# Kernel tuning notes

Hardware: AMD Instinct MI355X
Metric: run time of the kernel (lower is better)

## Reference

```python
import jax, jax.numpy as jnp
import numpy as np

N, E, B = 30000, 360000, 8
FN, FE, D, L, M = 64, 16, 128, 3, 8
DK = D // M
NEG_SLOPE = 0.2
EPS = 1e-5


def setup_inputs() -> dict:
    key = jax.random.key(0)
    ks = jax.random.split(key, 24)
    rng = np.random.default_rng(0)
    Ng, Eg = N // B, E // B
    off = np.repeat(np.arange(B, dtype=np.int64) * Ng, Eg)
    src = jnp.asarray(rng.integers(0, Ng, size=E) + off, dtype=jnp.int32)
    dst = jnp.asarray(rng.integers(0, Ng, size=E) + off, dtype=jnp.int32)
    node_graph = jnp.asarray(np.repeat(np.arange(B), Ng), dtype=jnp.int32)
    edge_graph = jnp.asarray(np.repeat(np.arange(B), Eg), dtype=jnp.int32)
    p = lambda i, *s: jax.random.normal(ks[i], s, jnp.float32) * 0.05
    return dict(
        h=jax.random.normal(ks[0], (N, FN), jnp.float32),
        e=jax.random.normal(ks[1], (E, FE), jnp.float32),
        src=src, dst=dst, node_graph=node_graph, edge_graph=edge_graph,
        emb_n_w=p(2, D, FN), emb_n_b=p(3, D),
        emb_e_w=p(4, D, FE), emb_e_b=p(5, D),
        Us=p(6, L, D, D), Vs=p(7, L, D, D), As=p(8, L, D, D),
        Bs=p(9, L, D, D), Cs=p(10, L, D, D),
        gat_src_w=p(11, M * DK, D), gat_src_b=p(12, M * DK),
        gat_dst_w=p(13, M * DK, D), gat_dst_b=p(14, M * DK),
        gat_attn=p(15, M, DK), gat_bias=p(16, M * DK),
        O_w=p(17, D, D), O_b=p(18, D),
        W1_w=p(19, D, 3 * D), W1_b=p(20, D),
        W2_w=p(21, 1, D), W2_b=p(22, 1))


def _bn(x):
    # BatchNorm1d(affine=False), training mode: biased variance over batch dim
    return (x - x.mean(0)) * jax.lax.rsqrt(x.var(0) + EPS)


def reference(h, e, src, dst, node_graph, edge_graph,
              emb_n_w, emb_n_b, emb_e_w, emb_e_b,
              Us, Vs, As, Bs, Cs,
              gat_src_w, gat_src_b, gat_dst_w, gat_dst_b, gat_attn, gat_bias,
              O_w, O_b, W1_w, W1_b, W2_w, W2_b):
    h = h @ emb_n_w.T + emb_n_b  # [N, D]
    e = e @ emb_e_w.T + emb_e_b  # [E, D]
    for l in range(L):
        # u_mul_e('h','w','m') + max('m','agg'): gather-mul-segment_max
        m = (h @ Vs[l].T)[src] * jax.nn.sigmoid(e)  # [E, D]
        agg = jax.ops.segment_max(m, dst, num_segments=N)
        agg = jnp.where(jnp.isneginf(agg), 0.0, agg)  # DGL fills zero-in-degree with 0
        h_new = h + jax.nn.relu(_bn(h @ Us[l].T + agg))
        # inc('in')^T @ B(h) = B(h)[dst]; inc('out')^T @ C(h) = C(h)[src] (uses pre-update h)
        ee = (h @ Bs[l].T)[dst] + (h @ Cs[l].T)[src]
        e = e + jax.nn.relu(_bn(e @ As[l].T + ee))
        h = h_new
    # GATv2Conv(D, DK, M heads, allow_zero_in_degree=True)
    fs = (h @ gat_src_w.T + gat_src_b).reshape(N, M, DK)
    fd = (h @ gat_dst_w.T + gat_dst_b).reshape(N, M, DK)
    z = jax.nn.leaky_relu(fs[src] + fd[dst], NEG_SLOPE)  # [E, M, DK]
    score = jnp.einsum('emk,mk->em', z, gat_attn)        # [E, M]
    smax = jax.ops.segment_max(score, dst, num_segments=N)[dst]
    p = jnp.exp(score - smax)
    denom = jax.ops.segment_sum(p, dst, num_segments=N)[dst]
    a = p / denom
    rst = jax.ops.segment_sum(a[:, :, None] * fs[src], dst, num_segments=N)
    rst = rst + gat_bias.reshape(1, M, DK)
    h = rst.reshape(N, D) @ O_w.T + O_b
    # per-graph mean of node states, broadcast to that graph's edges
    cnt = jax.ops.segment_sum(jnp.ones((N,), h.dtype), node_graph, num_segments=B)
    moy = jax.ops.segment_sum(h, node_graph, num_segments=B) / cnt[:, None]
    out = jnp.concatenate([moy[edge_graph], h[src], h[dst]], axis=1)  # [E, 3D]
    out = jax.nn.relu(out @ W1_w.T + W1_b)
    out = out @ W2_w.T + W2_b
    return jax.nn.sigmoid(out)[:, 0]
```

## Files before the change

kernel.cpp:

```cpp
#include <hip/hip_runtime.h>

#define DF 128
#define NGRAPH 8

typedef __attribute__((ext_vector_type(8))) short bf16x8;
typedef __attribute__((ext_vector_type(4))) float f32x4;

__device__ __forceinline__ float sigm(float x) { return 1.f / (1.f + __expf(-x)); }
__device__ __forceinline__ unsigned short f2bf(float f) {
  unsigned u = __float_as_uint(f);
  u += 0x7FFFu + ((u >> 16) & 1u);
  return (unsigned short)(u >> 16);
}
__device__ __forceinline__ float bf2f(unsigned short u) {
  return __uint_as_float(((unsigned)u) << 16);
}
__device__ __forceinline__ float bflo(unsigned u) { return __uint_as_float(u << 16); }
__device__ __forceinline__ float bfhi(unsigned u) { return __uint_as_float(u & 0xffff0000u); }

__device__ __forceinline__ bf16x8 cvt8(const float* __restrict__ p) {
  float4 a = *(const float4*)p;
  float4 b = *(const float4*)(p + 4);
  bf16x8 r;
  r[0] = (short)f2bf(a.x); r[1] = (short)f2bf(a.y);
// ... 3 lines not shown
  return r;
}

__device__ __forceinline__ void agg_max(unsigned hv, unsigned ev, float& m0, float& m1) {
  m0 = fmaxf(m0, bflo(hv) * sigm(bflo(ev)));
  m1 = fmaxf(m1, bfhi(hv) * sigm(bfhi(ev)));
}

__global__ void k_fill_u32(unsigned* __restrict__ p, unsigned v, long long n) {
  long long i = (long long)blockIdx.x * blockDim.x + threadIdx.x;
  long long st = (long long)gridDim.x * blockDim.x;
  for (; i < n; i += st) p[i] = v;
}

__global__ void k_deg(const int* __restrict__ dst, unsigned* __restrict__ deg, int E) {
  int i = blockIdx.x * blockDim.x + threadIdx.x;
  int st = gridDim.x * blockDim.x;
  for (; i < E; i += st) atomicAdd(&deg[dst[i]], 1u);
}

__global__ __launch_bounds__(1024) void k_scan(
    const unsigned* __restrict__ deg, unsigned* __restrict__ rowptr,
    unsigned* __restrict__ cursor, int N) {
  __shared__ unsigned part[1024];
  int t = threadIdx.x;
  int per = (N + 1023) >> 10;
  int s0 = t * per, s1 = min(N, s0 + per);
  unsigned s = 0;
  for (int i = s0; i < s1; ++i) s += deg[i];
  part[t] = s;
  __syncthreads();
  for (int off = 1; off < 1024; off <<= 1) {
    unsigned v = (t >= off) ? part[t - off] : 0u;
    __syncthreads();
    part[t] += v;
    __syncthreads();
  }
  unsigned base = (t == 0) ? 0u : part[t - 1];
  for (int i = s0; i < s1; ++i) {
    rowptr[i] = base;
    cursor[i] = base;
    base += deg[i];
  }
  if (t == 1023) rowptr[N] = part[1023];
}

__global__ void k_scatter(const int* __restrict__ dst, unsigned* __restrict__ cursor,
                          int* __restrict__ eidb, int E) {
  int i = blockIdx.x * blockDim.x + threadIdx.x;
  int st = gridDim.x * blockDim.x;
  for (; i < E; i += st) {
    unsigned p = atomicAdd(&cursor[dst[i]], 1u);
    eidb[p] = i;
  }
}

__global__ __launch_bounds__(512) void k_wconv(
    const float* __restrict__ Us, const float* __restrict__ Vs,
    const float* __restrict__ As, const float* __restrict__ Bs,
    const float* __restrict__ Cs, const float* __restrict__ gsw,
    const float* __restrict__ gdw, const float* __restrict__ Ow,
    const float* __restrict__ W1, short* __restrict__ out) {
  int b = blockIdx.x;
  const float* W;
  int ldw = DF;
  if (b < 3) W = Us + b * 16384;
  else if (b < 6) W = Vs + (b - 3) * 16384;
  else if (b < 9) W = As + (b - 6) * 16384;
  else if (b < 12) W = Bs + (b - 9) * 16384;
  else if (b < 15) W = Cs + (b - 12) * 16384;
  else if (b == 15) W = gsw;
  else if (b == 16) W = gdw;
  else if (b == 17) W = Ow;
  else if (b == 18) { W = W1 + 128; ldw = 384; }
  else { W = W1 + 256; ldw = 384; }
  short* o = out + (size_t)b * 2048 * 8;
  for (int s = threadIdx.x; s < 2048; s += 512) {
    int ct = s >> 8, ks = (s >> 6) & 3, l = s & 63;
    int row = ct * 16 + (l & 15), k0 = ks * 32 + (l >> 4) * 8;
    *(bf16x8*)&o[s * 8] = cvt8(W + (size_t)row * ldw + k0);
  }
}

__global__ __launch_bounds__(128) void k_node_embed(
    const float* __restrict__ hin, const float* __restrict__ w,
    const float* __restrict__ b, float* __restrict__ h0, int rows) {
  __shared__ float Wt[64 * DF];
  __shared__ float ar[4][64];
  int tid = threadIdx.x;
  for (int i = tid; i < 64 * DF; i += 128) Wt[(i & 63) * DF + (i >> 6)] = w[i];
  float bb = b[tid];
  __syncthreads();
  for (int r0 = blockIdx.x * 4; r0 < rows; r0 += gridDim.x * 4) {
    for (int i = tid; i < 256; i += 128) ar[i >> 6][i & 63] = hin[(size_t)r0 * 64 + i];
    __syncthreads();
    float a0 = bb, a1 = bb, a2 = bb, a3 = bb;
#pragma unroll 8
    for (int k = 0; k < 64; ++k) {
      float wv = Wt[k * DF + tid];
      a0 = fmaf(ar[0][k], wv, a0); a1 = fmaf(ar[1][k], wv, a1);
      a2 = fmaf(ar[2][k], wv, a2); a3 = fmaf(ar[3][k], wv, a3);
    }
    h0[(size_t)r0 * DF + tid] = a0;
    h0[(size_t)(r0 + 1) * DF + tid] = a1;
    h0[(size_t)(r0 + 2) * DF + tid] = a2;
    h0[(size_t)(r0 + 3) * DF + tid] = a3;
    __syncthreads();
  }
}

__global__ __launch_bounds__(128) void k_edge_embed(
    const float* __restrict__ ein, const float* __restrict__ w,
    const float* __restrict__ b, unsigned short* __restrict__ e0u, int rows) {
  __shared__ float Wt[16 * DF];
  __shared__ float ar[4][16];
  int tid = threadIdx.x;
  for (int i = tid; i < 16 * DF; i += 128) Wt[(i & 15) * DF + (i >> 4)] = w[i];
  float bb = b[tid];
  __syncthreads();
  for (int r0 = blockIdx.x * 4; r0 < rows; r0 += gridDim.x * 4) {
    if (tid < 64) ar[tid >> 4][tid & 15] = ein[(size_t)r0 * 16 + tid];
    __syncthreads();
    float a0 = bb, a1 = bb, a2 = bb, a3 = bb;
#pragma unroll
    for (int k = 0; k < 16; ++k) {
      float wv = Wt[k * DF + tid];
      a0 = fmaf(ar[0][k], wv, a0); a1 = fmaf(ar[1][k], wv, a1);
      a2 = fmaf(ar[2][k], wv, a2); a3 = fmaf(ar[3][k], wv, a3);
    }
    e0u[(size_t)r0 * DF + tid] = f2bf(a0);
    e0u[(size_t)(r0 + 1) * DF + tid] = f2bf(a1);
    e0u[(size_t)(r0 + 2) * DF + tid] = f2bf(a2);
    e0u[(size_t)(r0 + 3) * DF + tid] = f2bf(a3);
    __syncthreads();
  }
}

template <int OUTBF>
__global__ __launch_bounds__(512) void k_gemm_mfma(
    const float* __restrict__ A, const short* __restrict__ Wf,
    const float* __restrict__ bias, void* __restrict__ outv, int rows) {
  __shared__ short Wb[2048 * 8];
  int tid = threadIdx.x;
  for (int s = tid; s < 2048; s += 512)
    *(bf16x8*)&Wb[s * 8] = *(const bf16x8*)&Wf[(size_t)s * 8];
  __syncthreads();
  float* outf = (float*)outv;
  unsigned short* outb = (unsigned short*)outv;
  int wid = tid >> 6, lane = tid & 63, q = lane >> 4, m = lane & 15;
  int ntiles = (rows + 127) >> 7;
  for (int t = blockIdx.x; t < ntiles; t += gridDim.x) {
    int r0 = t * 128 + wid * 16;
    int rr = r0 + m;
    if (rr >= rows) rr = rows - 1;
    const float* ap = A + (size_t)rr * DF + q * 8;
    bf16x8 a[4];
#pragma unroll
    for (int ks = 0; ks < 4; ++ks) a[ks] = cvt8(ap + 32 * ks);
#pragma unroll
    for (int ct = 0; ct < 8; ++ct) {
      f32x4 acc = {0.f, 0.f, 0.f, 0.f};
#pragma unroll
      for (int ks = 0; ks < 4; ++ks) {
        bf16x8 b = *(const bf16x8*)&Wb[((ct * 4 + ks) * 64 + lane) * 8];
        acc = __builtin_amdgcn_mfma_f32_16x16x32_bf16(a[ks], b, acc, 0, 0, 0);
      }
      int col = ct * 16 + m;
      float bb = bias ? bias[col] : 0.f;
#pragma unroll
      for (int j = 0; j < 4; ++j) {
        int row = r0 + q * 4 + j;
        if (row < rows) {
          if (OUTBF) outb[(size_t)row * DF + col] = f2bf(acc[j] + bb);
          else outf[(size_t)row * DF + col] = acc[j] + bb;
// ... 41 lines not shown

__global__ __launch_bounds__(512) void k_gemm4_mfma(
    const float* __restrict__ h0, const short* __restrict__ Vf,
    const short* __restrict__ Uf, const short* __restrict__ Bf,
    const short* __restrict__ Cf, unsigned short* __restrict__ hVb,
    float* __restrict__ hU, unsigned short* __restrict__ hBb,
    unsigned short* __restrict__ hCb, int rows) {
  __shared__ short Wl[4 * 2048 * 8];
  int tid = threadIdx.x;
  for (int s = tid; s < 2048; s += 512) {
    *(bf16x8*)&Wl[(size_t)s * 8] = *(const bf16x8*)&Vf[(size_t)s * 8];
    *(bf16x8*)&Wl[(size_t)(2048 + s) * 8] = *(const bf16x8*)&Uf[(size_t)s * 8];
    *(bf16x8*)&Wl[(size_t)(4096 + s) * 8] = *(const bf16x8*)&Bf[(size_t)s * 8];
    *(bf16x8*)&Wl[(size_t)(6144 + s) * 8] = *(const bf16x8*)&Cf[(size_t)s * 8];
  }
  __syncthreads();
  int wid = tid >> 6, lane = tid & 63, q = lane >> 4, m = lane & 15;
  int ntiles = (rows + 127) >> 7;
  for (int t = blockIdx.x; t < ntiles; t += gridDim.x) {
    int r0 = t * 128 + wid * 16;
    int rr = r0 + m;
    if (rr >= rows) rr = rows - 1;
    const float* ap = h0 + (size_t)rr * DF + q * 8;
    bf16x8 a[4];
#pragma unroll
    for (int ks = 0; ks < 4; ++ks) a[ks] = cvt8(ap + 32 * ks);
#pragma unroll
    for (int w = 0; w < 4; ++w) {
#pragma unroll
      for (int ct = 0; ct < 8; ++ct) {
        f32x4 acc = {0.f, 0.f, 0.f, 0.f};
#pragma unroll
        for (int ks = 0; ks < 4; ++ks) {
          bf16x8 b = *(const bf16x8*)&Wl[((w * 2048) + (ct * 4 + ks) * 64 + lane) * 8];
          acc = __builtin_amdgcn_mfma_f32_16x16x32_bf16(a[ks], b, acc, 0, 0, 0);
        }
        int col = ct * 16 + m;
#pragma unroll
        for (int j = 0; j < 4; ++j) {
          int row = r0 + q * 4 + j;
          if (row < rows) {
            if (w == 1) hU[(size_t)row * DF + col] = acc[j];
            else {
              unsigned short v = f2bf(acc[j]);
              unsigned short* o = (w == 0) ? hVb : ((w == 2) ? hBb : hCb);
              o[(size_t)row * DF + col] = v;
            }
          }
        }
      }
    }
  }
}


#define EDGE_MFMA_BODY                                                                 \
  const unsigned short* ep = e0u + (size_t)ec * DF + q * 8;                            \
  bf16x8 bv0 = *(const bf16x8*)(ep);                                                   \
  bf16x8 bv1 = *(const bf16x8*)(ep + 32);                                              \
  bf16x8 bv2 = *(const bf16x8*)(ep + 64);                                              \
  bf16x8 bv3 = *(const bf16x8*)(ep + 96);                                              \
  f32x4 c0 = {0.f, 0.f, 0.f, 0.f}, c1 = c0, c2 = c0, c3 = c0;                          \
  f32x4 c4 = c0, c5 = c0, c6 = c0, c7 = c0;                                            \
  _Pragma("unroll") for (int ks = 0; ks < 4; ++ks) {                                   \
    bf16x8 bv = (ks == 0) ? bv0 : (ks == 1) ? bv1 : (ks == 2) ? bv2 : bv3;             \
    c0 = __builtin_amdgcn_mfma_f32_16x16x32_bf16(*(const bf16x8*)&Wb[((0 * 4 + ks) * 64 + lane) * 8], bv, c0, 0, 0, 0); \
    c1 = __builtin_amdgcn_mfma_f32_16x16x32_bf16(*(const bf16x8*)&Wb[((1 * 4 + ks) * 64 + lane) * 8], bv, c1, 0, 0, 0); \
    c2 = __builtin_amdgcn_mfma_f32_16x16x32_bf16(*(const bf16x8*)&Wb[((2 * 4 + ks) * 64 + lane) * 8], bv, c2, 0, 0, 0); \
    c3 = __builtin_amdgcn_mfma_f32_16x16x32_bf16(*(const bf16x8*)&Wb[((3 * 4 + ks) * 64 + lane) * 8], bv, c3, 0, 0, 0); \
    c4 = __builtin_amdgcn_mfma_f32_16x16x32_bf16(*(const bf16x8*)&Wb[((4 * 4 + ks) * 64 + lane) * 8], bv, c4, 0, 0, 0); \
    c5 = __builtin_amdgcn_mfma_f32_16x16x32_bf16(*(const bf16x8*)&Wb[((5 * 4 + ks) * 64 + lane) * 8], bv, c5, 0, 0, 0); \
    c6 = __builtin_amdgcn_mfma_f32_16x16x32_bf16(*(const bf16x8*)&Wb[((6 * 4 + ks) * 64 + lane) * 8], bv, c6, 0, 0, 0); \
    c7 = __builtin_amdgcn_mfma_f32_16x16x32_bf16(*(const bf16x8*)&Wb[((7 * 4 + ks) * 64 + lane) * 8], bv, c7, 0, 0, 0); \
  }

__global__ __launch_bounds__(512) void k_edge_xs(
    const unsigned short* __restrict__ e0u, const short* __restrict__ Af,
    const unsigned short* __restrict__ hBb, const unsigned short* __restrict__ hCb,
    const int* __restrict__ src, const int* __restrict__ dst,
    float* __restrict__ stat, int Eg) {
  __shared__ short Wb[2048 * 8];
  __shared__ float ls[256];
  int tid = threadIdx.x;
  for (int s = tid; s < 2048; s += 512)
    *(bf16x8*)&Wb[s * 8] = *(const bf16x8*)&Af[(size_t)s * 8];
  if (tid < 256) ls[tid] = 0.f;
  int wid = tid >> 6, lane = tid & 63, q = lane >> 4, m = lane & 15;
  int g = blockIdx.x & 7, sub = blockIdx.x >> 3, nsub = gridDim.x >> 3;
  int gbase = g * Eg, gend = gbase + Eg;
  int tpg = (Eg + 127) >> 7;
  float ps[32], pq[32];
#pragma unroll
  for (int i = 0; i < 32; ++i) { ps[i] = 0.f; pq[i] = 0.f; }
  __syncthreads();
  for (int t = sub; t < tpg; t += nsub) {
    int r0 = gbase + t * 128 + wid * 16;
    int edge = r0 + m;
    bool ok = edge < gend;
    int ec = ok ? edge : gend - 1;
    EDGE_MFMA_BODY
    if (ok) {
      int sidx = src[ec], didx = dst[ec];
      const unsigned short* pb = hBb + (size_t)didx * DF + q * 4;
      const unsigned short* pc = hCb + (size_t)sidx * DF + q * 4;
#pragma unroll
      for (int ct = 0; ct < 8; ++ct) {
        f32x4 cc = (ct == 0) ? c0 : (ct == 1) ? c1 : (ct == 2) ? c2 : (ct == 3) ? c3
                   : (ct == 4) ? c4 : (ct == 5) ? c5 : (ct == 6) ? c6 : c7;
        ushort4 hb = *(const ushort4*)(pb + ct * 16);
        ushort4 hc = *(const ushort4*)(pc + ct * 16);
        float x0 = cc[0] + bf2f(hb.x) + bf2f(hc.x);
        float x1 = cc[1] + bf2f(hb.y) + bf2f(hc.y);
        float x2 = cc[2] + bf2f(hb.z) + bf2f(hc.z);
        float x3 = cc[3] + bf2f(hb.w) + bf2f(hc.w);
        ps[ct * 4 + 0] += x0; pq[ct * 4 + 0] += x0 * x0;
        ps[ct * 4 + 1] += x1; pq[ct * 4 + 1] += x1 * x1;
        ps[ct * 4 + 2] += x2; pq[ct * 4 + 2] += x2 * x2;
        ps[ct * 4 + 3] += x3; pq[ct * 4 + 3] += x3 * x3;
      }
    }
  }
#pragma unroll
  for (int i = 0; i < 32; ++i) {
    float s = ps[i], sq = pq[i];
    s += __shfl_xor(s, 1, 64); sq += __shfl_xor(sq, 1, 64);
    s += __shfl_xor(s, 2, 64); sq += __shfl_xor(sq, 2, 64);
    s += __shfl_xor(s, 4, 64); sq += __shfl_xor(sq, 4, 64);
    s += __shfl_xor(s, 8, 64); sq += __shfl_xor(sq, 8, 64);
    if (m == 0) {
      int feat = (i >> 2) * 16 + q * 4 + (i & 3);
      atomicAdd(&ls[feat], s);
      atomicAdd(&ls[128 + feat], sq);
    }
  }
  __syncthreads();
  if (tid < 128) {
    atomicAdd(&stat[512 + tid], ls[tid]);
    atomicAdd(&stat[640 + tid], ls[128 + tid]);
  }
}

__global__ __launch_bounds__(512) void k_edge_xa(
    unsigned short* __restrict__ e0u, const short* __restrict__ Af,
    const unsigned short* __restrict__ hBb, const unsigned short* __restrict__ hCb,
    const int* __restrict__ src, const int* __restrict__ dst,
    const float* __restrict__ stat, int Eg) {
  __shared__ short Wb[2048 * 8];
  int tid = threadIdx.x;
  for (int s = tid; s < 2048; s += 512)
    *(bf16x8*)&Wb[s * 8] = *(const bf16x8*)&Af[(size_t)s * 8];
  int wid = tid >> 6, lane = tid & 63, q = lane >> 4, m = lane & 15;
  float mm[32], iv[32];
#pragma unroll
  for (int ct = 0; ct < 8; ++ct)
#pragma unroll
    for (int j = 0; j < 4; ++j) {
      int f = ct * 16 + q * 4 + j;
      mm[ct * 4 + j] = stat[768 + f];
      iv[ct * 4 + j] = stat[896 + f];
    }
  int g = blockIdx.x & 7, sub = blockIdx.x >> 3, nsub = gridDim.x >> 3;
  int gbase = g * Eg, gend = gbase + Eg;
  int tpg = (Eg + 127) >> 7;
  __syncthreads();
  for (int t = sub; t < tpg; t += nsub) {
    int r0 = gbase + t * 128 + wid * 16;
    int edge = r0 + m;
    bool ok = edge < gend;
    int ec = ok ? edge : gend - 1;
    EDGE_MFMA_BODY
    if (ok) {
      int sidx = src[ec], didx = dst[ec];
      const unsigned short* pb = hBb + (size_t)didx * DF + q * 4;
      const unsigned short* pc = hCb + (size_t)sidx * DF + q * 4;
      unsigned short* pe = e0u + (size_t)ec * DF + q * 4;
#pragma unroll
      for (int ct = 0; ct < 8; ++ct) {
        f32x4 cc = (ct == 0) ? c0 : (ct == 1) ? c1 : (ct == 2) ? c2 : (ct == 3) ? c3
                   : (ct == 4) ? c4 : (ct == 5) ? c5 : (ct == 6) ? c6 : c7;
        ushort4 hb = *(const ushort4*)(pb + ct * 16);
        ushort4 hc = *(const ushort4*)(pc + ct * 16);
        ushort4 eo = *(const ushort4*)(pe + ct * 16);
        float x0 = cc[0] + bf2f(hb.x) + bf2f(hc.x);
        float x1 = cc[1] + bf2f(hb.y) + bf2f(hc.y);
        float x2 = cc[2] + bf2f(hb.z) + bf2f(hc.z);
        float x3 = cc[3] + bf2f(hb.w) + bf2f(hc.w);
        ushort4 nv;
        nv.x = f2bf(bf2f(eo.x) + fmaxf((x0 - mm[ct * 4 + 0]) * iv[ct * 4 + 0], 0.f));
        nv.y = f2bf(bf2f(eo.y) + fmaxf((x1 - mm[ct * 4 + 1]) * iv[ct * 4 + 1], 0.f));
        nv.z = f2bf(bf2f(eo.z) + fmaxf((x2 - mm[ct * 4 + 2]) * iv[ct * 4 + 2], 0.f));
        nv.w = f2bf(bf2f(eo.w) + fmaxf((x3 - mm[ct * 4 + 3]) * iv[ct * 4 + 3], 0.f));
        *(ushort4*)(pe + ct * 16) = nv;
      }
    }
  }
}

__global__ __launch_bounds__(256) void k_node_agg(
    float* __restrict__ hU, const unsigned short* __restrict__ hVb,
    const unsigned short* __restrict__ e0u, const int* __restrict__ src,
    const unsigned* __restrict__ rowptr, const int* __restrict__ eidb,
    float* __restrict__ stat, int Ngr) {
  __shared__ float sr[4][256];
  int tid = threadIdx.x, wid = tid >> 6, lane = tid & 63;
  int g = blockIdx.x & 7, sub = blockIdx.x >> 3, nsub = gridDim.x >> 3;
  float ps0 = 0.f, ps1 = 0.f, pq0 = 0.f, pq1 = 0.f;
  for (int nn = sub * 4 + wid; nn < Ngr; nn += nsub * 4) {
    int n = g * Ngr + nn;
    unsigned r0 = rowptr[n], r1 = rowptr[n + 1];
    float m0 = -3.4e38f, m1 = -3.4e38f;
    for (unsigned rc = r0; rc < r1; rc += 64) {
      int batch = (int)min(64u, r1 - rc);
      int myE = eidb[rc + ((lane < batch) ? lane : 0)];
      int myS = src[myE];
      int j = 0;
      for (; j + 4 <= batch; j += 4) {
        int e0 = __shfl(myE, j, 64), e1 = __shfl(myE, j + 1, 64);
        int e2 = __shfl(myE, j + 2, 64), e3 = __shfl(myE, j + 3, 64);
        int s0 = __shfl(myS, j, 64), s1 = __shfl(myS, j + 1, 64);
        int s2 = __shfl(myS, j + 2, 64), s3 = __shfl(myS, j + 3, 64);
        unsigned h0v = *(const unsigned*)&hVb[(size_t)s0 * DF + 2 * lane];
        unsigned h1v = *(const unsigned*)&hVb[(size_t)s1 * DF + 2 * lane];
        unsigned h2v = *(const unsigned*)&hVb[(size_t)s2 * DF + 2 * lane];
        unsigned h3v = *(const unsigned*)&hVb[(size_t)s3 * DF + 2 * lane];
        unsigned v0 = *(const unsigned*)&e0u[(size_t)e0 * DF + 2 * lane];
        unsigned v1 = *(const unsigned*)&e0u[(size_t)e1 * DF + 2 * lane];
        unsigned v2 = *(const unsigned*)&e0u[(size_t)e2 * DF + 2 * lane];
        unsigned v3 = *(const unsigned*)&e0u[(size_t)e3 * DF + 2 * lane];
        agg_max(h0v, v0, m0, m1);
        agg_max(h1v, v1, m0, m1);
        agg_max(h2v, v2, m0, m1);
        agg_max(h3v, v3, m0, m1);
      }
      for (; j < batch; ++j) {
        int e = __shfl(myE, j, 64);
        int s = __shfl(myS, j, 64);
        unsigned hv = *(const unsigned*)&hVb[(size_t)s * DF + 2 * lane];
        unsigned ev = *(const unsigned*)&e0u[(size_t)e * DF + 2 * lane];
        agg_max(hv, ev, m0, m1);
      }
    }
    if (r1 == r0) { m0 = 0.f; m1 = 0.f; }
    size_t idx = (size_t)n * DF + 2 * lane;
    float2 hu = *(float2*)&hU[idx];
    float t0 = hu.x + m0, t1 = hu.y + m1;
    hu.x = t0; hu.y = t1;
    *(float2*)&hU[idx] = hu;
    ps0 += t0; ps1 += t1;
    pq0 += t0 * t0; pq1 += t1 * t1;
  }
  sr[0][tid] = ps0; sr[1][tid] = ps1; sr[2][tid] = pq0; sr[3][tid] = pq1;
  __syncthreads();
  if (tid < 64) {
    float a0 = 0.f, a1 = 0.f, b0 = 0.f, b1 = 0.f;
#pragma unroll
    for (int w = 0; w < 4; ++w) {
      a0 += sr[0][w * 64 + tid]; a1 += sr[1][w * 64 + tid];
      b0 += sr[2][w * 64 + tid]; b1 += sr[3][w * 64 + tid];
    }
    atomicAdd(&stat[2 * tid], a0);
    atomicAdd(&stat[2 * tid + 1], a1);
    atomicAdd(&stat[128 + 2 * tid], b0);
    atomicAdd(&stat[128 + 2 * tid + 1], b1);
  }
}

__global__ void k_bn_finalize(float* __restrict__ stat, float nN, float nE) {
  int tid = threadIdx.x;
  if (tid < 128) {
    float mean = stat[tid] / nN;
    float var = stat[128 + tid] / nN - mean * mean;
    stat[256 + tid] = mean;
    stat[384 + tid] = rsqrtf(fmaxf(var, 0.f) + 1e-5f);
  } else {
    int d = tid - 128;
    float mean = stat[512 + d] / nE;
    float var = stat[640 + d] / nE - mean * mean;
    stat[768 + d] = mean;
    stat[896 + d] = rsqrtf(fmaxf(var, 0.f) + 1e-5f);
  }
}

__global__ __launch_bounds__(256) void k_node_update(
    float* __restrict__ h0, const float* __restrict__ hU,
    const float* __restrict__ stat, long long total) {
  long long i = (long long)blockIdx.x * blockDim.x + threadIdx.x;
  long long st = (long long)gridDim.x * blockDim.x;
  for (; i < total; i += st) {
    int d = (int)(i & 127);
    float t = (hU[i] - stat[256 + d]) * stat[384 + d];
    h0[i] += fmaxf(t, 0.f);
  }
}

__global__ __launch_bounds__(256) void k_gat_score(
    const unsigned short* __restrict__ fsb, const unsigned short* __restrict__ fdb,
    const int* __restrict__ src, const int* __restrict__ dst,
    const float* __restrict__ attn, float* __restrict__ score, int Eg) {
  int g = blockIdx.x & 7, sub = blockIdx.x >> 3, nsub = gridDim.x >> 3;
  int gbase = g * Eg, gend = gbase + Eg;
  int tpg = (Eg + 127) >> 7;
  int tid = threadIdx.x;
  for (int t = sub; t < tpg; t += nsub) {
    int ebase = gbase + t * 128;
    for (int k = tid; k < 1024; k += 256) {
      int e = ebase + (k >> 3);
      if (e >= gend) break;
      int mh = k & 7;
      int s = src[e], dn = dst[e];
      const unsigned short* ps = fsb + (size_t)s * DF + mh * 16;
      const unsigned short* pd = fdb + (size_t)dn * DF + mh * 16;
      const float* pa = attn + mh * 16;
      bf16x8 s0 = *(const bf16x8*)ps;
      bf16x8 s1 = *(const bf16x8*)(ps + 8);
      bf16x8 d0 = *(const bf16x8*)pd;
      bf16x8 d1 = *(const bf16x8*)(pd + 8);
      float acc = 0.f;
#pragma unroll
      for (int kk = 0; kk < 8; ++kk) {
        float z = bf2f((unsigned short)s0[kk]) + bf2f((unsigned short)d0[kk]);
        z = (z > 0.f) ? z : 0.2f * z;
        acc = fmaf(z, pa[kk], acc);
        float z2 = bf2f((unsigned short)s1[kk]) + bf2f((unsigned short)d1[kk]);
        z2 = (z2 > 0.f) ? z2 : 0.2f * z2;
        acc = fmaf(z2, pa[kk + 8], acc);
      }
      score[(size_t)e * 8 + mh] = acc;
    }
  }
}

__global__ __launch_bounds__(256) void k_gat_node(
    const float* __restrict__ score, const unsigned short* __restrict__ fsb,
    const int* __restrict__ src, const unsigned* __restrict__ rowptr,
    const int* __restrict__ eidb, float* __restrict__ rst, int Ngr) {
  int tid = threadIdx.x, wid = tid >> 6, lane = tid & 63;
  int g = blockIdx.x & 7, sub = blockIdx.x >> 3, nsub = gridDim.x >> 3;
  int head = lane >> 3, slot = lane & 7;
  for (int nn = sub * 4 + wid; nn < Ngr; nn += nsub * 4) {
    int n = g * Ngr + nn;
    unsigned r0 = rowptr[n], r1 = rowptr[n + 1];
    float hm = -3.4e38f;
    for (unsigned rc = r0; rc < r1; rc += 64) {
      int batch = (int)min(64u, r1 - rc);
      int myE = eidb[rc + ((lane < batch) ? lane : 0)];
      for (int k = slot; k < batch; k += 8) {
        int e = __shfl(myE, k, 64);
        hm = fmaxf(hm, score[(size_t)e * 8 + head]);
      }
    }
#pragma unroll
    for (int mk = 1; mk < 8; mk <<= 1) hm = fmaxf(hm, __shfl_xor(hm, mk, 64));
    float dn = 0.f;
    for (unsigned rc = r0; rc < r1; rc += 64) {
      int batch = (int)min(64u, r1 - rc);
      int myE = eidb[rc + ((lane < batch) ? lane : 0)];
      for (int k = slot; k < batch; k += 8) {
        int e = __shfl(myE, k, 64);
        dn += __expf(score[(size_t)e * 8 + head] - hm);
      }
    }
#pragma unroll
    for (int mk = 1; mk < 8; mk <<= 1) dn += __shfl_xor(dn, mk, 64);
    float inv = (r1 > r0) ? 1.f / dn : 0.f;
    float a0 = 0.f, a1 = 0.f;
    for (unsigned rc = r0; rc < r1; rc += 64) {
      int batch = (int)min(64u, r1 - rc);
      int myE = eidb[rc + ((lane < batch) ? lane : 0)];
      int myS = src[myE];
      int j = 0;
      for (; j + 4 <= batch; j += 4) {
        int e0 = __shfl(myE, j, 64), e1 = __shfl(myE, j + 1, 64);
        int e2 = __shfl(myE, j + 2, 64), e3 = __shfl(myE, j + 3, 64);
        int s0 = __shfl(myS, j, 64), s1 = __shfl(myS, j + 1, 64);
        int s2 = __shfl(myS, j + 2, 64), s3 = __shfl(myS, j + 3, 64);
        float sc0 = score[(size_t)e0 * 8 + head];
        float sc1 = score[(size_t)e1 * 8 + head];
        float sc2 = score[(size_t)e2 * 8 + head];
        float sc3 = score[(size_t)e3 * 8 + head];
        unsigned f0 = *(const unsigned*)&fsb[(size_t)s0 * DF + 2 * lane];
        unsigned f1 = *(const unsigned*)&fsb[(size_t)s1 * DF + 2 * lane];
        unsigned f2 = *(const unsigned*)&fsb[(size_t)s2 * DF + 2 * lane];
        unsigned f3 = *(const unsigned*)&fsb[(size_t)s3 * DF + 2 * lane];
        float w0 = __expf(sc0 - hm) * inv, w1 = __expf(sc1 - hm) * inv;
        float w2 = __expf(sc2 - hm) * inv, w3 = __expf(sc3 - hm) * inv;
        a0 = fmaf(w0, bflo(f0), a0); a1 = fmaf(w0, bfhi(f0), a1);
        a0 = fmaf(w1, bflo(f1), a0); a1 = fmaf(w1, bfhi(f1), a1);
        a0 = fmaf(w2, bflo(f2), a0); a1 = fmaf(w2, bfhi(f2), a1);
        a0 = fmaf(w3, bflo(f3), a0); a1 = fmaf(w3, bfhi(f3), a1);
      }
      for (; j < batch; ++j) {
        int e = __shfl(myE, j, 64);
        int s = __shfl(myS, j, 64);
        float w = __expf(score[(size_t)e * 8 + head] - hm) * inv;
        unsigned fv = *(const unsigned*)&fsb[(size_t)s * DF + 2 * lane];
        a0 = fmaf(w, bflo(fv), a0);
        a1 = fmaf(w, bfhi(fv), a1);
      }
    }
    float2 o;
    o.x = a0; o.y = a1;
    *(float2*)&rst[(size_t)n * DF + 2 * lane] = o;
  }
}

__global__ void k_bias2(const float* __restrict__ gat_bias,
                        const float* __restrict__ O_w,
                        const float* __restrict__ O_b, float* __restrict__ bias2) {
  int d = threadIdx.x;
  float acc = O_b[d];
  for (int k = 0; k < DF; ++k) acc = fmaf(gat_bias[k], O_w[(size_t)d * DF + k], acc);
  bias2[d] = acc;
}

__global__ __launch_bounds__(128) void k_moy(
    const unsigned short* __restrict__ h2b, const int* __restrict__ ng,
    float* __restrict__ moy, float* __restrict__ cnt, int rows) {
  int tid = threadIdx.x;
  int per = (rows + gridDim.x - 1) / gridDim.x;
  int n0 = blockIdx.x * per;
  int n1 = min(rows, n0 + per);
  if (n0 >= n1) return;
  int cur = ng[n0];
  float acc = 0.f; int c = 0;
  for (int n = n0; n < n1; ++n) {
    int g = ng[n];
    if (g != cur) {
      atomicAdd(&moy[cur * DF + tid], acc);
      if (tid == 0) atomicAdd(&cnt[cur], (float)c);
      acc = 0.f; c = 0; cur = g;
    }
    acc += bf2f(h2b[(size_t)n * DF + tid]);
    ++c;
  }
  atomicAdd(&moy[cur * DF + tid], acc);
  if (tid == 0) atomicAdd(&cnt[cur], (float)c);
}

__global__ void k_p0(const float* __restrict__ W1, const float* __restrict__ W1b_,
                     const float* __restrict__ moy, const float* __restrict__ cnt,
                     float* __restrict__ P0) {
  int g = blockIdx.x, d = threadIdx.x;
  float inv = 1.f / cnt[g];
  float acc = W1b_[d];
  for (int k = 0; k < DF; ++k) acc = fmaf(W1[(size_t)d * 384 + k], moy[g * DF + k] * inv, acc);
  P0[g * DF + d] = acc;
}

__global__ __launch_bounds__(256) void k_head(
    const unsigned short* __restrict__ P1b, const unsigned short* __restrict__ P2b,
    const float* __restrict__ P0, const int* __restrict__ src,
    const unsigned* __restrict__ rowptr, const int* __restrict__ eidb,
    const float* __restrict__ W2, const float* __restrict__ W2b,
    float* __restrict__ out, int Ngr) {
  int tid = threadIdx.x, wid = tid >> 6, lane = tid & 63;
  int g = blockIdx.x & 7, sub = blockIdx.x >> 3, nsub = gridDim.x >> 3;
  float w2b = W2b[0];
  float w20 = W2[2 * lane], w21 = W2[2 * lane + 1];
  float b0 = P0[g * DF + 2 * lane], b1v = P0[g * DF + 2 * lane + 1];
  for (int nn = sub * 4 + wid; nn < Ngr; nn += nsub * 4) {
    int n = g * Ngr + nn;
    unsigned r0 = rowptr[n], r1 = rowptr[n + 1];
    if (r1 == r0) continue;
    unsigned p2 = *(const unsigned*)&P2b[(size_t)n * DF + 2 * lane];
    float base0 = b0 + bflo(p2);
    float base1 = b1v + bfhi(p2);
    for (unsigned rc = r0; rc < r1; rc += 64) {
      int cnt2 = (int)min(64u, r1 - rc);
      int myE = eidb[rc + ((lane < cnt2) ? lane : 0)];
      int myS = src[myE];
      int j = 0;
      for (; j + 4 <= cnt2; j += 4) {
        int e0 = __shfl(myE, j, 64), e1 = __shfl(myE, j + 1, 64);
        int e2 = __shfl(myE, j + 2, 64), e3 = __shfl(myE, j + 3, 64);
        int s0 = __shfl(myS, j, 64), s1 = __shfl(myS, j + 1, 64);
        int s2 = __shfl(myS, j + 2, 64), s3 = __shfl(myS, j + 3, 64);
        unsigned u0 = *(const unsigned*)&P1b[(size_t)s0 * DF + 2 * lane];
        unsigned u1 = *(const unsigned*)&P1b[(size_t)s1 * DF + 2 * lane];
        unsigned u2 = *(const unsigned*)&P1b[(size_t)s2 * DF + 2 * lane];
        unsigned u3 = *(const unsigned*)&P1b[(size_t)s3 * DF + 2 * lane];
        float v0 = fmaxf(base0 + bflo(u0), 0.f) * w20 + fmaxf(base1 + bfhi(u0), 0.f) * w21;
        float v1 = fmaxf(base0 + bflo(u1), 0.f) * w20 + fmaxf(base1 + bfhi(u1), 0.f) * w21;
        float v2 = fmaxf(base0 + bflo(u2), 0.f) * w20 + fmaxf(base1 + bfhi(u2), 0.f) * w21;
        float v3 = fmaxf(base0 + bflo(u3), 0.f) * w20 + fmaxf(base1 + bfhi(u3), 0.f) * w21;
#pragma unroll
        for (int mk = 1; mk < 64; mk <<= 1) {
          v0 += __shfl_xor(v0, mk, 64);
          v1 += __shfl_xor(v1, mk, 64);
          v2 += __shfl_xor(v2, mk, 64);
          v3 += __shfl_xor(v3, mk, 64);
        }
        if (lane == 0) {
          out[e0] = sigm(v0 + w2b);
          out[e1] = sigm(v1 + w2b);
          out[e2] = sigm(v2 + w2b);
          out[e3] = sigm(v3 + w2b);
        }
      }
      for (; j < cnt2; ++j) {
        int e = __shfl(myE, j, 64);
        int s = __shfl(myS, j, 64);
        unsigned p1 = *(const unsigned*)&P1b[(size_t)s * DF + 2 * lane];
        float v = fmaxf(base0 + bflo(p1), 0.f) * w20 + fmaxf(base1 + bfhi(p1), 0.f) * w21;
#pragma unroll
        for (int mk = 1; mk < 64; mk <<= 1) v += __shfl_xor(v, mk, 64);
        if (lane == 0) out[e] = sigm(v + w2b);
      }
    }
  }
}

extern "C" void kernel_launch(void* const* d_in, const int* in_sizes, int n_in,
                              void* d_out, int out_size, void* d_ws, size_t ws_size,
                              hipStream_t stream) {
  const float* h_in = (const float*)d_in[0];
  const float* e_in = (const float*)d_in[1];
  const int* src = (const int*)d_in[2];
  const int* dst = (const int*)d_in[3];
  const int* node_graph = (const int*)d_in[4];
  const float* emb_n_w = (const float*)d_in[6];
  const float* emb_n_b = (const float*)d_in[7];
  const float* emb_e_w = (const float*)d_in[8];
  const float* emb_e_b = (const float*)d_in[9];
  const float* Us = (const float*)d_in[10];
  const float* Vs = (const float*)d_in[11];
  const float* As = (const float*)d_in[12];
  const float* Bs = (const float*)d_in[13];
  const float* Cs = (const float*)d_in[14];
  const float* gat_src_w = (const float*)d_in[15];
  const float* gat_src_b = (const float*)d_in[16];
  const float* gat_dst_w = (const float*)d_in[17];
  const float* gat_dst_b = (const float*)d_in[18];
  const float* gat_attn = (const float*)d_in[19];
  const float* gat_bias = (const float*)d_in[20];
  const float* O_w = (const float*)d_in[21];
  const float* O_b = (const float*)d_in[22];
  const float* W1_w = (const float*)d_in[23];
  const float* W1_b = (const float*)d_in[24];
  const float* W2_w = (const float*)d_in[25];
  const float* W2_b = (const float*)d_in[26];
  float* out = (float*)d_out;

  const int N = in_sizes[0] / 64;
  const int E = in_sizes[1] / 16;
  const int Eg = E / NGRAPH;
  const int Ngr = N / NGRAPH;

  auto rnd = [](size_t b) { return (b + 255) & ~(size_t)255; };
  const size_t sz_e0 = rnd((size_t)E * DF * 2);
  const size_t sz_node = rnd((size_t)N * DF * 4);
  const size_t sz_nodeb = rnd((size_t)N * DF * 2);
  const size_t sz_score = rnd((size_t)E * 8 * 4);
  const size_t sz_wfrag = rnd(20 * 2048 * 8 * 2);
  const size_t sz_rp = rnd((size_t)(N + 1) * 4);
  const size_t sz_eid = rnd((size_t)E * 4);
  const size_t sz_misc = rnd(4096 * 4);
  const size_t needed = sz_e0 + 3 * sz_node + 4 * sz_nodeb + sz_score + sz_wfrag +
                        3 * sz_rp + sz_eid + sz_misc;
  if (ws_size < needed) {
    k_fill_u32<<<256, 256, 0, stream>>>((unsigned*)out, 0xBF800000u, (long long)out_size);
    return;
  }

  char* wp = (char*)d_ws;
  auto alloc = [&](size_t bytes) { void* p = wp; wp += bytes; return p; };
  unsigned short* e0u = (unsigned short*)alloc(sz_e0);
  float* h0 = (float*)alloc(sz_node);
  float* hU = (float*)alloc(sz_node);
  float* rst = (float*)alloc(sz_node);
  unsigned short* hVb = (unsigned short*)alloc(sz_nodeb);
  unsigned short* hBb = (unsigned short*)alloc(sz_nodeb);
  unsigned short* hCb = (unsigned short*)alloc(sz_nodeb);
  unsigned short* h2b = (unsigned short*)alloc(sz_nodeb);
  float* score = (float*)alloc(sz_score);
  short* wfrag = (short*)alloc(sz_wfrag);
  unsigned* rowptr = (unsigned*)alloc(sz_rp);
  unsigned* cursor = (unsigned*)alloc(sz_rp);
  unsigned* deg = (unsigned*)alloc(sz_rp);
  int* eidb = (int*)alloc(sz_eid);
  float* misc = (float*)alloc(sz_misc);
  float* stat = misc;
  float* bias2 = misc + 1024;
  float* moy = misc + 1152;
  float* cnt = misc + 2176;
  float* P0 = misc + 2304;
  unsigned short* P1b = e0u;
  unsigned short* P2b = e0u + (size_t)N * DF;

  auto WF = [&](int idx) { return wfrag + (size_t)idx * 2048 * 8; };

  k_fill_u32<<<64, 256, 0, stream>>>(deg, 0u, N);
  k_deg<<<512, 256, 0, stream>>>(dst, deg, E);
  k_scan<<<1, 1024, 0, stream>>>(deg, rowptr, cursor, N);
  k_scatter<<<512, 256, 0, stream>>>(dst, cursor, eidb, E);

  k_wconv<<<20, 512, 0, stream>>>(Us, Vs, As, Bs, Cs, gat_src_w, gat_dst_w, O_w,
                                  W1_w, wfrag);

  const int gN = (N + 127) / 128;
  k_node_embed<<<2048, 128, 0, stream>>>(h_in, emb_n_w, emb_n_b, h0, N);
  k_edge_embed<<<4096, 128, 0, stream>>>(e_in, emb_e_w, emb_e_b, e0u, E);

  for (int l = 0; l < 3; ++l) {
    k_gemm4_mfma<<<gN, 512, 0, stream>>>(h0, WF(3 + l), WF(l), WF(9 + l), WF(12 + l),
                                         hVb, hU, hBb, hCb, N);
    k_fill_u32<<<4, 256, 0, stream>>>((unsigned*)stat, 0u, 1024);
    k_node_agg<<<2048, 256, 0, stream>>>(hU, hVb, e0u, src, rowptr, eidb, stat, Ngr);
    k_edge_xs<<<1024, 512, 0, stream>>>(e0u, WF(6 + l), hBb, hCb, src, dst, stat, Eg);
    k_bn_finalize<<<1, 256, 0, stream>>>(stat, (float)N, (float)E);
    k_node_update<<<2048, 256, 0, stream>>>(h0, hU, stat, (long long)N * DF);
    k_edge_xa<<<1024, 512, 0, stream>>>(e0u, WF(6 + l), hBb, hCb, src, dst, stat, Eg);
  }

  k_gemm_mfma<1><<<gN, 512, 0, stream>>>(h0, WF(15), gat_src_b, hVb, N);
  k_gemm_mfma<1><<<gN, 512, 0, stream>>>(h0, WF(16), gat_dst_b, hBb, N);
  k_gat_score<<<512, 256, 0, stream>>>(hVb, hBb, src, dst, gat_attn, score, Eg);
  k_gat_node<<<2048, 256, 0, stream>>>(score, hVb, src, rowptr, eidb, rst, Ngr);
  k_bias2<<<1, 128, 0, stream>>>(gat_bias, O_w, O_b, bias2);
  k_gemm_mfma<1><<<gN, 512, 0, stream>>>(rst, WF(17), bias2, h2b, N);

  k_fill_u32<<<2, 256, 0, stream>>>((unsigned*)moy, 0u, 1032);
  k_moy<<<128, 128, 0, stream>>>(h2b, node_graph, moy, cnt, N);
  k_p0<<<8, 128, 0, stream>>>(W1_w, W1_b, moy, cnt, P0);
  k_gemmb_mfma<<<gN, 512, 0, stream>>>(h2b, WF(18), P1b, N);
  k_gemmb_mfma<<<gN, 512, 0, stream>>>(h2b, WF(19), P2b, N);
  k_head<<<2048, 256, 0, stream>>>(P1b, P2b, P0, src, rowptr, eidb, W2_w, W2_b,
                                   out, Ngr);
}
```

Baseline: 1.473 ms.

## Store edge state in destination-sorted order with permuted src/dst indices

Edge embeddings are now written in CSR (destination-sorted) order, and permuted src/dst index arrays are built once, so the node aggregation, GAT softmax and edge kernels read edge data contiguously instead of through the eidb indirection. This removes a random gather per edge in node_agg and gat_node, and the GAT score kernel is flattened into a simple grid-stride loop. The cost is one extra permutation kernel, two more index buffers, and a gathered read of the raw edge features during embedding. Per-graph edge ranges still hold because edges stay within their graph after sorting.

```diff
diff --git a/kernel.cpp b/kernel.cpp
--- a/kernel.cpp
+++ b/kernel.cpp
@@ -79,6 +79,18 @@
   for (; i < E; i += st) {
     unsigned p = atomicAdd(&cursor[dst[i]], 1u);
     eidb[p] = i;
+  }
+}
+
+__global__ void k_permidx(const int* __restrict__ eidb, const int* __restrict__ src,
+                          const int* __restrict__ dst, int* __restrict__ srcP,
+                          int* __restrict__ dstP, int E) {
+  int i = blockIdx.x * blockDim.x + threadIdx.x;
+  int st = gridDim.x * blockDim.x;
+  for (; i < E; i += st) {
+    int e = eidb[i];
+    srcP[i] = src[e];
+    dstP[i] = dst[e];
   }
 }
 
@@ -137,8 +149,9 @@
 }
 
 __global__ __launch_bounds__(128) void k_edge_embed(
-    const float* __restrict__ ein, const float* __restrict__ w,
-    const float* __restrict__ b, unsigned short* __restrict__ e0u, int rows) {
+    const float* __restrict__ ein, const int* __restrict__ eidb,
+    const float* __restrict__ w, const float* __restrict__ b,
+    unsigned short* __restrict__ e0u, int rows) {
   __shared__ float Wt[16 * DF];
   __shared__ float ar[4][16];
   int tid = threadIdx.x;
@@ -146,7 +159,10 @@
   float bb = b[tid];
   __syncthreads();
   for (int r0 = blockIdx.x * 4; r0 < rows; r0 += gridDim.x * 4) {
-    if (tid < 64) ar[tid >> 4][tid & 15] = ein[(size_t)r0 * 16 + tid];
+    if (tid < 64) {
+      int e = eidb[r0 + (tid >> 4)];
+      ar[tid >> 4][tid & 15] = ein[(size_t)e * 16 + (tid & 15)];
+    }
     __syncthreads();
     float a0 = bb, a1 = bb, a2 = bb, a3 = bb;
 #pragma unroll
@@ -294,7 +310,6 @@
     }
   }
 }
-
 
 #define EDGE_MFMA_BODY                                                                 \
   const unsigned short* ep = e0u + (size_t)ec * DF + q * 8;                            \
@@ -319,7 +334,7 @@
 __global__ __launch_bounds__(512) void k_edge_xs(
     const unsigned short* __restrict__ e0u, const short* __restrict__ Af,
     const unsigned short* __restrict__ hBb, const unsigned short* __restrict__ hCb,
-    const int* __restrict__ src, const int* __restrict__ dst,
+    const int* __restrict__ srcP, const int* __restrict__ dstP,
     float* __restrict__ stat, int Eg) {
   __shared__ short Wb[2048 * 8];
   __shared__ float ls[256];
@@ -342,7 +357,7 @@
     int ec = ok ? edge : gend - 1;
     EDGE_MFMA_BODY
     if (ok) {
-      int sidx = src[ec], didx = dst[ec];
+      int sidx = srcP[ec], didx = dstP[ec];
       const unsigned short* pb = hBb + (size_t)didx * DF + q * 4;
       const unsigned short* pc = hCb + (size_t)sidx * DF + q * 4;
 #pragma unroll
@@ -385,7 +400,7 @@
 __global__ __launch_bounds__(512) void k_edge_xa(
     unsigned short* __restrict__ e0u, const short* __restrict__ Af,
     const unsigned short* __restrict__ hBb, const unsigned short* __restrict__ hCb,
-    const int* __restrict__ src, const int* __restrict__ dst,
+    const int* __restrict__ srcP, const int* __restrict__ dstP,
     const float* __restrict__ stat, int Eg) {
   __shared__ short Wb[2048 * 8];
   int tid = threadIdx.x;
@@ -412,7 +427,7 @@
     int ec = ok ? edge : gend - 1;
     EDGE_MFMA_BODY
     if (ok) {
-      int sidx = src[ec], didx = dst[ec];
+      int sidx = srcP[ec], didx = dstP[ec];
       const unsigned short* pb = hBb + (size_t)didx * DF + q * 4;
       const unsigned short* pc = hCb + (size_t)sidx * DF + q * 4;
       unsigned short* pe = e0u + (size_t)ec * DF + q * 4;
@@ -440,9 +455,8 @@
 
 __global__ __launch_bounds__(256) void k_node_agg(
     float* __restrict__ hU, const unsigned short* __restrict__ hVb,
-    const unsigned short* __restrict__ e0u, const int* __restrict__ src,
-    const unsigned* __restrict__ rowptr, const int* __restrict__ eidb,
-    float* __restrict__ stat, int Ngr) {
+    const unsigned short* __restrict__ e0u, const int* __restrict__ srcP,
+    const unsigned* __restrict__ rowptr, float* __restrict__ stat, int Ngr) {
   __shared__ float sr[4][256];
   int tid = threadIdx.x, wid = tid >> 6, lane = tid & 63;
   int g = blockIdx.x & 7, sub = blockIdx.x >> 3, nsub = gridDim.x >> 3;
@@ -453,32 +467,28 @@
     float m0 = -3.4e38f, m1 = -3.4e38f;
     for (unsigned rc = r0; rc < r1; rc += 64) {
       int batch = (int)min(64u, r1 - rc);
-      int myE = eidb[rc + ((lane < batch) ? lane : 0)];
-      int myS = src[myE];
+      int myS = srcP[rc + ((lane < batch) ? lane : 0)];
       int j = 0;
       for (; j + 4 <= batch; j += 4) {
-        int e0 = __shfl(myE, j, 64), e1 = __shfl(myE, j + 1, 64);
-        int e2 = __shfl(myE, j + 2, 64), e3 = __shfl(myE, j + 3, 64);
         int s0 = __shfl(myS, j, 64), s1 = __shfl(myS, j + 1, 64);
         int s2 = __shfl(myS, j + 2, 64), s3 = __shfl(myS, j + 3, 64);
         unsigned h0v = *(const unsigned*)&hVb[(size_t)s0 * DF + 2 * lane];
         unsigned h1v = *(const unsigned*)&hVb[(size_t)s1 * DF + 2 * lane];
         unsigned h2v = *(const unsigned*)&hVb[(size_t)s2 * DF + 2 * lane];
         unsigned h3v = *(const unsigned*)&hVb[(size_t)s3 * DF + 2 * lane];
-        unsigned v0 = *(const unsigned*)&e0u[(size_t)e0 * DF + 2 * lane];
-        unsigned v1 = *(const unsigned*)&e0u[(size_t)e1 * DF + 2 * lane];
-        unsigned v2 = *(const unsigned*)&e0u[(size_t)e2 * DF + 2 * lane];
-        unsigned v3 = *(const unsigned*)&e0u[(size_t)e3 * DF + 2 * lane];
+        unsigned v0 = *(const unsigned*)&e0u[(size_t)(rc + j) * DF + 2 * lane];
+        unsigned v1 = *(const unsigned*)&e0u[(size_t)(rc + j + 1) * DF + 2 * lane];
+        unsigned v2 = *(const unsigned*)&e0u[(size_t)(rc + j + 2) * DF + 2 * lane];
+        unsigned v3 = *(const unsigned*)&e0u[(size_t)(rc + j + 3) * DF + 2 * lane];
         agg_max(h0v, v0, m0, m1);
         agg_max(h1v, v1, m0, m1);
         agg_max(h2v, v2, m0, m1);
         agg_max(h3v, v3, m0, m1);
       }
       for (; j < batch; ++j) {
-        int e = __shfl(myE, j, 64);
         int s = __shfl(myS, j, 64);
         unsigned hv = *(const unsigned*)&hVb[(size_t)s * DF + 2 * lane];
-        unsigned ev = *(const unsigned*)&e0u[(size_t)e * DF + 2 * lane];
+        unsigned ev = *(const unsigned*)&e0u[(size_t)(rc + j) * DF + 2 * lane];
         agg_max(hv, ev, m0, m1);
       }
     }
@@ -537,45 +547,39 @@
 
 __global__ __launch_bounds__(256) void k_gat_score(
     const unsigned short* __restrict__ fsb, const unsigned short* __restrict__ fdb,
-    const int* __restrict__ src, const int* __restrict__ dst,
-    const float* __restrict__ attn, float* __restrict__ score, int Eg) {
-  int g = blockIdx.x & 7, sub = blockIdx.x >> 3, nsub = gridDim.x >> 3;
-  int gbase = g * Eg, gend = gbase + Eg;
-  int tpg = (Eg + 127) >> 7;
-  int tid = threadIdx.x;
-  for (int t = sub; t < tpg; t += nsub) {
-    int ebase = gbase + t * 128;
-    for (int k = tid; k < 1024; k += 256) {
-      int e = ebase + (k >> 3);
-      if (e >= gend) break;
-      int mh = k & 7;
-      int s = src[e], dn = dst[e];
-      const unsigned short* ps = fsb + (size_t)s * DF + mh * 16;
-      const unsigned short* pd = fdb + (size_t)dn * DF + mh * 16;
-      const float* pa = attn + mh * 16;
-      bf16x8 s0 = *(const bf16x8*)ps;
-      bf16x8 s1 = *(const bf16x8*)(ps + 8);
-      bf16x8 d0 = *(const bf16x8*)pd;
-      bf16x8 d1 = *(const bf16x8*)(pd + 8);
-      float acc = 0.f;
-#pragma unroll
-      for (int kk = 0; kk < 8; ++kk) {
-        float z = bf2f((unsigned short)s0[kk]) + bf2f((unsigned short)d0[kk]);
-        z = (z > 0.f) ? z : 0.2f * z;
-        acc = fmaf(z, pa[kk], acc);
-        float z2 = bf2f((unsigned short)s1[kk]) + bf2f((unsigned short)d1[kk]);
-        z2 = (z2 > 0.f) ? z2 : 0.2f * z2;
-        acc = fmaf(z2, pa[kk + 8], acc);
-      }
-      score[(size_t)e * 8 + mh] = acc;
-    }
+    const int* __restrict__ srcP, const int* __restrict__ dstP,
+    const float* __restrict__ attn, float* __restrict__ score, int E) {
+  long long i = (long long)blockIdx.x * blockDim.x + threadIdx.x;
+  long long st = (long long)gridDim.x * blockDim.x;
+  long long total = (long long)E * 8;
+  for (; i < total; i += st) {
+    int e = (int)(i >> 3), mh = (int)(i & 7);
+    int s = srcP[e], dn = dstP[e];
+    const unsigned short* ps = fsb + (size_t)s * DF + mh * 16;
+    const unsigned short* pd = fdb + (size_t)dn * DF + mh * 16;
+    const float* pa = attn + mh * 16;
+    bf16x8 s0 = *(const bf16x8*)ps;
+    bf16x8 s1 = *(const bf16x8*)(ps + 8);
+    bf16x8 d0 = *(const bf16x8*)pd;
+    bf16x8 d1 = *(const bf16x8*)(pd + 8);
+    float acc = 0.f;
+#pragma unroll
+    for (int kk = 0; kk < 8; ++kk) {
+      float z = bf2f((unsigned short)s0[kk]) + bf2f((unsigned short)d0[kk]);
+      z = (z > 0.f) ? z : 0.2f * z;
+      acc = fmaf(z, pa[kk], acc);
+      float z2 = bf2f((unsigned short)s1[kk]) + bf2f((unsigned short)d1[kk]);
+      z2 = (z2 > 0.f) ? z2 : 0.2f * z2;
+      acc = fmaf(z2, pa[kk + 8], acc);
+    }
+    score[i] = acc;
   }
 }
 
 __global__ __launch_bounds__(256) void k_gat_node(
     const float* __restrict__ score, const unsigned short* __restrict__ fsb,
-    const int* __restrict__ src, const unsigned* __restrict__ rowptr,
-    const int* __restrict__ eidb, float* __restrict__ rst, int Ngr) {
+    const int* __restrict__ srcP, const unsigned* __restrict__ rowptr,
+    float* __restrict__ rst, int Ngr) {
   int tid = threadIdx.x, wid = tid >> 6, lane = tid & 63;
   int g = blockIdx.x & 7, sub = blockIdx.x >> 3, nsub = gridDim.x >> 3;
   int head = lane >> 3, slot = lane & 7;
@@ -583,43 +587,28 @@
     int n = g * Ngr + nn;
     unsigned r0 = rowptr[n], r1 = rowptr[n + 1];
     float hm = -3.4e38f;
-    for (unsigned rc = r0; rc < r1; rc += 64) {
-      int batch = (int)min(64u, r1 - rc);
-      int myE = eidb[rc + ((lane < batch) ? lane : 0)];
-      for (int k = slot; k < batch; k += 8) {
-        int e = __shfl(myE, k, 64);
-        hm = fmaxf(hm, score[(size_t)e * 8 + head]);
-      }
-    }
+    for (unsigned r = r0 + slot; r < r1; r += 8)
+      hm = fmaxf(hm, score[(size_t)r * 8 + head]);
 #pragma unroll
     for (int mk = 1; mk < 8; mk <<= 1) hm = fmaxf(hm, __shfl_xor(hm, mk, 64));
     float dn = 0.f;
-    for (unsigned rc = r0; rc < r1; rc += 64) {
-      int batch = (int)min(64u, r1 - rc);
-      int myE = eidb[rc + ((lane < batch) ? lane : 0)];
-      for (int k = slot; k < batch; k += 8) {
-        int e = __shfl(myE, k, 64);
-        dn += __expf(score[(size_t)e * 8 + head] - hm);
-      }
-    }
+    for (unsigned r = r0 + slot; r < r1; r += 8)
+      dn += __expf(score[(size_t)r * 8 + head] - hm);
 #pragma unroll
     for (int mk = 1; mk < 8; mk <<= 1) dn += __shfl_xor(dn, mk, 64);
     float inv = (r1 > r0) ? 1.f / dn : 0.f;
     float a0 = 0.f, a1 = 0.f;
     for (unsigned rc = r0; rc < r1; rc += 64) {
       int batch = (int)min(64u, r1 - rc);
-      int myE = eidb[rc + ((lane < batch) ? lane : 0)];
-      int myS = src[myE];
+      int myS = srcP[rc + ((lane < batch) ? lane : 0)];
       int j = 0;
       for (; j + 4 <= batch; j += 4) {
-        int e0 = __shfl(myE, j, 64), e1 = __shfl(myE, j + 1, 64);
-        int e2 = __shfl(myE, j + 2, 64), e3 = __shfl(myE, j + 3, 64);
         int s0 = __shfl(myS, j, 64), s1 = __shfl(myS, j + 1, 64);
         int s2 = __shfl(myS, j + 2, 64), s3 = __shfl(myS, j + 3, 64);
-        float sc0 = score[(size_t)e0 * 8 + head];
-        float sc1 = score[(size_t)e1 * 8 + head];
-        float sc2 = score[(size_t)e2 * 8 + head];
-        float sc3 = score[(size_t)e3 * 8 + head];
+        float sc0 = score[(size_t)(rc + j) * 8 + head];
+        float sc1 = score[(size_t)(rc + j + 1) * 8 + head];
+        float sc2 = score[(size_t)(rc + j + 2) * 8 + head];
+        float sc3 = score[(size_t)(rc + j + 3) * 8 + head];
         unsigned f0 = *(const unsigned*)&fsb[(size_t)s0 * DF + 2 * lane];
         unsigned f1 = *(const unsigned*)&fsb[(size_t)s1 * DF + 2 * lane];
         unsigned f2 = *(const unsigned*)&fsb[(size_t)s2 * DF + 2 * lane];
@@ -632,9 +621,8 @@
         a0 = fmaf(w3, bflo(f3), a0); a1 = fmaf(w3, bfhi(f3), a1);
       }
       for (; j < batch; ++j) {
-        int e = __shfl(myE, j, 64);
         int s = __shfl(myS, j, 64);
-        float w = __expf(score[(size_t)e * 8 + head] - hm) * inv;
+        float w = __expf(score[(size_t)(rc + j) * 8 + head] - hm) * inv;
         unsigned fv = *(const unsigned*)&fsb[(size_t)s * DF + 2 * lane];
         a0 = fmaf(w, bflo(fv), a0);
         a1 = fmaf(w, bfhi(fv), a1);
@@ -691,7 +679,7 @@
 
 __global__ __launch_bounds__(256) void k_head(
     const unsigned short* __restrict__ P1b, const unsigned short* __restrict__ P2b,
-    const float* __restrict__ P0, const int* __restrict__ src,
+    const float* __restrict__ P0, const int* __restrict__ srcP,
     const unsigned* __restrict__ rowptr, const int* __restrict__ eidb,
     const float* __restrict__ W2, const float* __restrict__ W2b,
     float* __restrict__ out, int Ngr) {
@@ -710,7 +698,7 @@
     for (unsigned rc = r0; rc < r1; rc += 64) {
       int cnt2 = (int)min(64u, r1 - rc);
       int myE = eidb[rc + ((lane < cnt2) ? lane : 0)];
-      int myS = src[myE];
+      int myS = srcP[rc + ((lane < cnt2) ? lane : 0)];
       int j = 0;
       for (; j + 4 <= cnt2; j += 4) {
         int e0 = __shfl(myE, j, 64), e1 = __shfl(myE, j + 1, 64);
@@ -798,7 +786,7 @@
   const size_t sz_eid = rnd((size_t)E * 4);
   const size_t sz_misc = rnd(4096 * 4);
   const size_t needed = sz_e0 + 3 * sz_node + 4 * sz_nodeb + sz_score + sz_wfrag +
-                        3 * sz_rp + sz_eid + sz_misc;
+                        3 * sz_rp + 3 * sz_eid + sz_misc;
   if (ws_size < needed) {
     k_fill_u32<<<256, 256, 0, stream>>>((unsigned*)out, 0xBF800000u, (long long)out_size);
     return;
@@ -820,6 +808,8 @@
   unsigned* cursor = (unsigned*)alloc(sz_rp);
   unsigned* deg = (unsigned*)alloc(sz_rp);
   int* eidb = (int*)alloc(sz_eid);
+  int* srcP = (int*)alloc(sz_eid);
+  int* dstP = (int*)alloc(sz_eid);
   float* misc = (float*)alloc(sz_misc);
   float* stat = misc;
   float* bias2 = misc + 1024;
@@ -835,29 +825,30 @@
   k_deg<<<512, 256, 0, stream>>>(dst, deg, E);
   k_scan<<<1, 1024, 0, stream>>>(deg, rowptr, cursor, N);
   k_scatter<<<512, 256, 0, stream>>>(dst, cursor, eidb, E);
+  k_permidx<<<512, 256, 0, stream>>>(eidb, src, dst, srcP, dstP, E);
 
   k_wconv<<<20, 512, 0, stream>>>(Us, Vs, As, Bs, Cs, gat_src_w, gat_dst_w, O_w,
                                   W1_w, wfrag);
 
   const int gN = (N + 127) / 128;
   k_node_embed<<<2048, 128, 0, stream>>>(h_in, emb_n_w, emb_n_b, h0, N);
-  k_edge_embed<<<4096, 128, 0, stream>>>(e_in, emb_e_w, emb_e_b, e0u, E);
+  k_edge_embed<<<4096, 128, 0, stream>>>(e_in, eidb, emb_e_w, emb_e_b, e0u, E);
 
   for (int l = 0; l < 3; ++l) {
     k_gemm4_mfma<<<gN, 512, 0, stream>>>(h0, WF(3 + l), WF(l), WF(9 + l), WF(12 + l),
                                          hVb, hU, hBb, hCb, N);
     k_fill_u32<<<4, 256, 0, stream>>>((unsigned*)stat, 0u, 1024);
-    k_node_agg<<<2048, 256, 0, stream>>>(hU, hVb, e0u, src, rowptr, eidb, stat, Ngr);
-    k_edge_xs<<<1024, 512, 0, stream>>>(e0u, WF(6 + l), hBb, hCb, src, dst, stat, Eg);
+    k_node_agg<<<2048, 256, 0, stream>>>(hU, hVb, e0u, srcP, rowptr, stat, Ngr);
+    k_edge_xs<<<1024, 512, 0, stream>>>(e0u, WF(6 + l), hBb, hCb, srcP, dstP, stat, Eg);
     k_bn_finalize<<<1, 256, 0, stream>>>(stat, (float)N, (float)E);
     k_node_update<<<2048, 256, 0, stream>>>(h0, hU, stat, (long long)N * DF);
-    k_edge_xa<<<1024, 512, 0, stream>>>(e0u, WF(6 + l), hBb, hCb, src, dst, stat, Eg);
+    k_edge_xa<<<1024, 512, 0, stream>>>(e0u, WF(6 + l), hBb, hCb, srcP, dstP, stat, Eg);
   }
 
   k_gemm_mfma<1><<<gN, 512, 0, stream>>>(h0, WF(15), gat_src_b, hVb, N);
   k_gemm_mfma<1><<<gN, 512, 0, stream>>>(h0, WF(16), gat_dst_b, hBb, N);
-  k_gat_score<<<512, 256, 0, stream>>>(hVb, hBb, src, dst, gat_attn, score, Eg);
-  k_gat_node<<<2048, 256, 0, stream>>>(score, hVb, src, rowptr, eidb, rst, Ngr);
+  k_gat_score<<<2048, 256, 0, stream>>>(hVb, hBb, srcP, dstP, gat_attn, score, E);
+  k_gat_node<<<2048, 256, 0, stream>>>(score, hVb, srcP, rowptr, rst, Ngr);
   k_bias2<<<1, 128, 0, stream>>>(gat_bias, O_w, O_b, bias2);
   k_gemm_mfma<1><<<gN, 512, 0, stream>>>(rst, WF(17), bias2, h2b, N);
 
@@ -866,6 +857,6 @@
   k_p0<<<8, 128, 0, stream>>>(W1_w, W1_b, moy, cnt, P0);
   k_gemmb_mfma<<<gN, 512, 0, stream>>>(h2b, WF(18), P1b, N);
   k_gemmb_mfma<<<gN, 512, 0, stream>>>(h2b, WF(19), P2b, N);
-  k_head<<<2048, 256, 0, stream>>>(P1b, P2b, P0, src, rowptr, eidb, W2_w, W2_b,
+  k_head<<<2048, 256, 0, stream>>>(P1b, P2b, P0, srcP, rowptr, eidb, W2_w, W2_b,
                                    out, Ngr);
 }
```

Measured after the change: 1.388 ms, median of 2. 1.06x faster.
